# Performance work log

Hardware: AMD Instinct MI355X
Metric: run time of the kernel (lower is better)

Reference implementation:

```python
import jax, jax.numpy as jnp
import numpy as np

WH, WW = 8, 8            # window_size
N_TOK = WH * WW          # tokens per window = 64
DIM = 128
HEADS = 4
HEAD_DIM = DIM // HEADS  # 32
B_WIN = 4096             # batch * num_windows
EPS = 1e-6


def _swin_relative_index():
    # standard Swin relative_position_index, shape (N, N), values in [0, (2Wh-1)*(2Ww-1))
    coords = np.stack(np.meshgrid(np.arange(WH), np.arange(WW), indexing='ij'))  # (2, Wh, Ww)
    coords = coords.reshape(2, -1)                                               # (2, N)
    rel = coords[:, :, None] - coords[:, None, :]                                # (2, N, N)
    rel = rel.transpose(1, 2, 0).astype(np.int32)                                # (N, N, 2)
    rel[..., 0] += WH - 1
    rel[..., 1] += WW - 1
    rel[..., 0] *= 2 * WW - 1
    return rel.sum(-1)                                                           # (N, N)


def _coords_grid():
    # normalized relative coordinate table, shape ((2Wh-1)*(2Ww-1), 2) in [-1, 1]
    rh = np.arange(-(WH - 1), WH, dtype=np.float32) / max(WH - 1, 1)
    rw = np.arange(-(WW - 1), WW, dtype=np.float32) / max(WW - 1, 1)
    return np.stack(np.meshgrid(rh, rw, indexing='ij'), -1).reshape(-1, 2)


def setup_inputs() -> dict:
    key = jax.random.key(0)
    ks = jax.random.split(key, 8)
    s = 0.02
    return {
        'x':       jax.random.normal(ks[0], (B_WIN, N_TOK, DIM), jnp.float32),
        'W_qkv':   jax.random.normal(ks[1], (DIM, 3 * DIM), jnp.float32) * s,
        'W_proj':  jax.random.normal(ks[2], (DIM, DIM), jnp.float32) * s,
        'b_proj':  jnp.zeros((DIM,), jnp.float32),
        'cpb_w1':  jax.random.normal(ks[3], (2, 512), jnp.float32) * s,
        'cpb_b1':  jnp.zeros((512,), jnp.float32),
        'cpb_w2':  jax.random.normal(ks[4], (512, HEADS), jnp.float32) * s,
        'h_times':   jnp.float32(2.0),
        'pow_para':  jnp.float32(0.0),
        'ws_scalar': jnp.float32(1.0),
        'ws_scalar2': jnp.float32(2.0),
        'rel_index': jnp.asarray(_swin_relative_index()),          # (N, N) int32
        'coords':    jnp.asarray(_coords_grid()),                  # (225, 2) float32
    }


def reference(x, W_qkv, W_proj, b_proj, cpb_w1, cpb_b1, cpb_w2,
              h_times, pow_para, ws_scalar, ws_scalar2, rel_index, coords):
    B, N, C = x.shape
    scale = HEAD_DIM ** -0.5

    # qkv projection (bias=False), split into heads
    qkv = (x @ W_qkv).reshape(B, N, 3, HEADS, HEAD_DIM)
    qkv = jnp.transpose(qkv, (2, 0, 3, 1, 4))           # (3, B, H, N, hd)
    q, k, v = qkv[0], qkv[1], qkv[2]

    attn = jnp.einsum('bhnd,bhmd->bhnm', q, k) * scale  # (B, H, N, N)

    # dynamic position bias: parametrized coord transform -> small MLP -> gather
    ht = jax.nn.softplus(h_times)
    pp = jax.nn.sigmoid(pow_para)
    ws = jax.nn.softplus(ws_scalar) / jax.nn.softplus(ws_scalar2)
    t = coords * ht                                      # (225, 2)
    t = jnp.sign(t) * (jnp.abs(t) + EPS) ** pp * ws      # pow_mode coord warp
    bias_table = jax.nn.relu(t @ cpb_w1 + cpb_b1) @ cpb_w2   # (225, H)
    bias = bias_table[rel_index]                         # (N, N, H)
    attn = attn + jnp.transpose(bias, (2, 0, 1))[None]   # (B, H, N, N)

    attn = jax.nn.softmax(attn, axis=-1)
    out = jnp.einsum('bhnm,bhmd->bnhd', attn, v).reshape(B, N, C)
    return out @ W_proj + b_proj
```

## Files before the change

### kernel.cpp

```cpp
#include <hip/hip_runtime.h>
#include <hip/hip_bf16.h>

typedef __hip_bfloat16 bf16;
typedef __bf16 bf8v __attribute__((ext_vector_type(8)));
typedef float f4v __attribute__((ext_vector_type(4)));

#define WS_BIAS   0
#define WS_TABLE  32768
#define WS_QKVT   36864
#define WS_PROJT  135168
#define WS_FLAG   167936

__device__ __forceinline__ float rdf(const void* p, int i, int isbf) {
  return isbf ? __bfloat162float(((const bf16*)p)[i]) : ((const float*)p)[i];
}

__global__ void detect_dtype(const unsigned short* __restrict__ coords_raw,
                             char* __restrict__ ws) {
  *(int*)(ws + WS_FLAG) = (coords_raw[0] != 0) ? 1 : 0;
}

__global__ void prep_transpose(const void* __restrict__ Wqkv,
                               const void* __restrict__ Wproj,
                               char* __restrict__ ws) {
  int idx = blockIdx.x * 256 + threadIdx.x;
  int isbf = *(const int*)(ws + WS_FLAG);
  bf16* qt = (bf16*)(ws + WS_QKVT);
  bf16* pt = (bf16*)(ws + WS_PROJT);
  if (idx < 384 * 128) {
    int c = idx >> 7, k = idx & 127;
    qt[idx] = __float2bfloat16(rdf(Wqkv, k * 384 + c, isbf));
  } else {
    int j = idx - 384 * 128;
    int c = j >> 7, k = j & 127;
    pt[j] = __float2bfloat16(rdf(Wproj, k * 128 + c, isbf));
  }
}

__global__ void prep_table(const void* __restrict__ coords,
                           const void* __restrict__ w1,
                           const void* __restrict__ b1,
                           const void* __restrict__ w2,
                           const void* __restrict__ hts,
                           const void* __restrict__ pps,
                           const void* __restrict__ ws1,
                           const void* __restrict__ ws2,
                           char* __restrict__ ws) {
  __shared__ float red[8][4];
  const int r = blockIdx.x;
  const int j = threadIdx.x;
  const int isbf = *(const int*)(ws + WS_FLAG);
  float* table = (float*)(ws + WS_TABLE);

  float ht  = log1pf(__expf(rdf(hts, 0, isbf)));
  float pp  = 1.f / (1.f + __expf(-rdf(pps, 0, isbf)));
  float wsv = log1pf(__expf(rdf(ws1, 0, isbf))) /
              log1pf(__expf(rdf(ws2, 0, isbf)));
  float t0 = rdf(coords, 2 * r + 0, isbf) * ht;
  float t1 = rdf(coords, 2 * r + 1, isbf) * ht;
  float s0 = (t0 > 0.f) ? 1.f : ((t0 < 0.f) ? -1.f : 0.f);
  float s1 = (t1 > 0.f) ? 1.f : ((t1 < 0.f) ? -1.f : 0.f);
  float u0 = s0 * __powf(fabsf(t0) + 1e-6f, pp) * wsv;
  float u1 = s1 * __powf(fabsf(t1) + 1e-6f, pp) * wsv;

  float h = u0 * rdf(w1, j, isbf) + u1 * rdf(w1, 512 + j, isbf) + rdf(b1, j, isbf);
  h = fmaxf(h, 0.f);
  float a[4];
#pragma unroll
  for (int q = 0; q < 4; ++q) a[q] = h * rdf(w2, 4 * j + q, isbf);
#pragma unroll
  for (int off = 1; off < 64; off <<= 1)
#pragma unroll
    for (int q = 0; q < 4; ++q) a[q] += __shfl_xor(a[q], off);
  int wv = j >> 6, ln = j & 63;
  if (ln == 0) {
#pragma unroll
    for (int q = 0; q < 4; ++q) red[wv][q] = a[q];
  }
  __syncthreads();
  if (j < 4) {
    float s = 0.f;
#pragma unroll
    for (int w8 = 0; w8 < 8; ++w8) s += red[w8][j];
    table[r * 4 + j] = s;
  }
}

__global__ void prep_gather(const int* __restrict__ rel, char* __restrict__ ws) {
  int pos = blockIdx.x * 256 + threadIdx.x;
  const float* table = (const float*)(ws + WS_TABLE);
  bf16* bias = (bf16*)(ws + WS_BIAS);
  int h = pos >> 10, rest = pos & 1023;
  int mt = rest >> 8, n4 = (rest >> 6) & 3, quad = (rest >> 4) & 3, l16 = rest & 15;
  int jj = n4 * 16 + l16;
  union { uint2 u; bf16 hh[4]; } pk;
#pragma unroll
  for (int r = 0; r < 4; ++r) {
    int i = mt * 16 + quad * 4 + r;
    int rr = rel[i * 64 + jj];
    pk.hh[r] = __float2bfloat16(table[rr * 4 + h]);
  }
  *(uint2*)(bias + pos * 4) = pk.u;
}

__global__ __launch_bounds__(256, 4) void wattn_main(
    const void* __restrict__ xp,
    const char* __restrict__ ws,
    const void* __restrict__ bprojp,
    void* __restrict__ outp) {
  __shared__ alignas(16) char smem[26624];
  bf16* xls = (bf16*)smem;
  bf16* os  = (bf16*)smem;
  const int tid  = threadIdx.x;
  const int w    = tid >> 6;
  const int lane = tid & 63;
  const int l16  = lane & 15;
  const int quad = lane >> 4;
  bf16* scr = (bf16*)(smem + 17408 + w * 2304);

  const int isbf = *(const int*)(ws + WS_FLAG);
  const bf16* WqkvT  = (const bf16*)(ws + WS_QKVT);
  const bf16* WprojT = (const bf16*)(ws + WS_PROJT);
  const bf16* biasg  = (const bf16*)(ws + WS_BIAS);

  const int b = blockIdx.x;

  if (isbf) {
    const bf16* xb = (const bf16*)xp + (size_t)b * 8192;
#pragma unroll
    for (int it = 0; it < 4; ++it) {
      int e = (tid + it * 256) * 8;
      int row = e >> 7, col = e & 127;
      *(uint4*)(xls + row * 136 + col) = *(const uint4*)(xb + e);
    }
  } else {
    const float* xb = (const float*)xp + (size_t)b * 8192;
#pragma unroll
    for (int it = 0; it < 4; ++it) {
      int e = (tid + it * 256) * 8;
      int row = e >> 7, col = e & 127;
      f4v a = *(const f4v*)(xb + e);
      f4v c = *(const f4v*)(xb + e + 4);
      union { uint4 u; bf16 h[8]; } pk;
#pragma unroll
      for (int jj = 0; jj < 4; ++jj) {
        pk.h[jj]     = __float2bfloat16(a[jj]);
        pk.h[4 + jj] = __float2bfloat16(c[jj]);
      }
      *(uint4*)(xls + row * 136 + col) = pk.u;
    }
  }
  __syncthreads();

  const f4v zf = {0.f, 0.f, 0.f, 0.f};
  bf8v vf[2][2], qf[4], kf[4];

  auto run_qkv = [&](int colbase, f4v (&acc)[4][2]) {
    const bf16* Bb = WqkvT + (size_t)colbase * 128;
#pragma unroll
    for (int ks = 0; ks < 4; ++ks) {
      bf8v xk[4];
#pragma unroll
      for (int mt = 0; mt < 4; ++mt)
        xk[mt] = *(const bf8v*)(xls + (mt * 16 + l16) * 136 + ks * 32 + quad * 8);
#pragma unroll
      for (int nt = 0; nt < 2; ++nt) {
        bf8v bfr = *(const bf8v*)(Bb + (nt * 16 + l16) * 128 + ks * 32 + quad * 8);
#pragma unroll
        for (int mt = 0; mt < 4; ++mt)
          acc[mt][nt] = __builtin_amdgcn_mfma_f32_16x16x32_bf16(xk[mt], bfr, acc[mt][nt], 0, 0, 0);
      }
    }
  };

  {
    f4v acc[4][2];
#pragma unroll
    for (int mt = 0; mt < 4; ++mt) { acc[mt][0] = zf; acc[mt][1] = zf; }
    run_qkv(256 + w * 32, acc);
#pragma unroll
    for (int nt = 0; nt < 2; ++nt) {
#pragma unroll
      for (int mt = 0; mt < 4; ++mt) {
        union { uint2 u; bf16 h[4]; } pk;
#pragma unroll
        for (int r = 0; r < 4; ++r) pk.h[r] = __float2bfloat16(acc[mt][nt][r]);
        *(uint2*)(scr + l16 * 72 + mt * 16 + quad * 4) = pk.u;
      }
#pragma unroll
      for (int k2 = 0; k2 < 2; ++k2)
        vf[k2][nt] = *(const bf8v*)(scr + l16 * 72 + k2 * 32 + quad * 8);
    }
  }

  {
    f4v acc[4][2];
#pragma unroll
    for (int mt = 0; mt < 4; ++mt) { acc[mt][0] = zf; acc[mt][1] = zf; }
    run_qkv(w * 32, acc);
#pragma unroll
    for (int mt = 0; mt < 4; ++mt) {
#pragma unroll
      for (int nt = 0; nt < 2; ++nt)
#pragma unroll
        for (int r = 0; r < 4; ++r)
          scr[(quad * 4 + r) * 40 + nt * 16 + l16] = __float2bfloat16(acc[mt][nt][r]);
      qf[mt] = *(const bf8v*)(scr + l16 * 40 + quad * 8);
    }
  }

  {
    f4v acc[4][2];
#pragma unroll
    for (int mt = 0; mt < 4; ++mt) { acc[mt][0] = zf; acc[mt][1] = zf; }
    run_qkv(128 + w * 32, acc);
#pragma unroll
    for (int mt = 0; mt < 4; ++mt) {
#pragma unroll
      for (int nt = 0; nt < 2; ++nt)
#pragma unroll
        for (int r = 0; r < 4; ++r)
          scr[(quad * 4 + r) * 40 + nt * 16 + l16] = __float2bfloat16(acc[mt][nt][r]);
      kf[mt] = *(const bf8v*)(scr + l16 * 40 + quad * 8);
    }
  }

  __syncthreads();

  const float scale = 0.1767766952966369f;
  const bf16* bh = biasg + w * 4096;
  for (int mt = 0; mt < 4; ++mt) {
    f4v sc[4];
#pragma unroll
    for (int n4 = 0; n4 < 4; ++n4)
      sc[n4] = __builtin_amdgcn_mfma_f32_16x16x32_bf16(qf[mt], kf[n4], zf, 0, 0, 0);
    float p[4][4];
#pragma unroll
    for (int n4 = 0; n4 < 4; ++n4) {
      union { uint2 u; bf16 hh[4]; } bb;
      bb.u = *(const uint2*)(bh + mt * 1024 + n4 * 256 + quad * 64 + l16 * 4);
#pragma unroll
      for (int r = 0; r < 4; ++r)
        p[n4][r] = sc[n4][r] * scale + __bfloat162float(bb.hh[r]);
    }
#pragma unroll
    for (int r = 0; r < 4; ++r) {
      float m = fmaxf(fmaxf(p[0][r], p[1][r]), fmaxf(p[2][r], p[3][r]));
      m = fmaxf(m, __shfl_xor(m, 1, 16));
      m = fmaxf(m, __shfl_xor(m, 2, 16));
      m = fmaxf(m, __shfl_xor(m, 4, 16));
      m = fmaxf(m, __shfl_xor(m, 8, 16));
      float s = 0.f;
#pragma unroll
      for (int n4 = 0; n4 < 4; ++n4) { p[n4][r] = __expf(p[n4][r] - m); s += p[n4][r]; }
      s += __shfl_xor(s, 1, 16);
      s += __shfl_xor(s, 2, 16);
      s += __shfl_xor(s, 4, 16);
      s += __shfl_xor(s, 8, 16);
      float inv = __builtin_amdgcn_rcpf(s);
#pragma unroll
      for (int n4 = 0; n4 < 4; ++n4) p[n4][r] *= inv;
    }
#pragma unroll
    for (int n4 = 0; n4 < 4; ++n4)
#pragma unroll
      for (int r = 0; r < 4; ++r)
        scr[(quad * 4 + r) * 72 + n4 * 16 + l16] = __float2bfloat16(p[n4][r]);

    f4v o2[2] = {zf, zf};
#pragma unroll
    for (int k2 = 0; k2 < 2; ++k2) {
      bf8v pf = *(const bf8v*)(scr + l16 * 72 + k2 * 32 + quad * 8);
#pragma unroll
      for (int nt = 0; nt < 2; ++nt)
        o2[nt] = __builtin_amdgcn_mfma_f32_16x16x32_bf16(pf, vf[k2][nt], o2[nt], 0, 0, 0);
    }
#pragma unroll
    for (int nt = 0; nt < 2; ++nt) {
      union { uint2 u; bf16 h[4]; } pk;
#pragma unroll
      for (int r = 0; r < 4; ++r) pk.h[r] = __float2bfloat16(o2[nt][r]);
#pragma unroll
      for (int r = 0; r < 4; ++r)
        os[(mt * 16 + quad * 4 + r) * 136 + w * 32 + nt * 16 + l16] = pk.h[r];
    }
  }

  __syncthreads();

  f4v pa[4][2];
#pragma unroll
  for (int mt = 0; mt < 4; ++mt) { pa[mt][0] = zf; pa[mt][1] = zf; }
#pragma unroll
  for (int ks = 0; ks < 4; ++ks) {
    bf8v oa[4];
#pragma unroll
    for (int mt = 0; mt < 4; ++mt)
      oa[mt] = *(const bf8v*)(os + (mt * 16 + l16) * 136 + ks * 32 + quad * 8);
#pragma unroll
    for (int nt = 0; nt < 2; ++nt) {
      bf8v bfr = *(const bf8v*)(WprojT + (size_t)(w * 32 + nt * 16 + l16) * 128 + ks * 32 + quad * 8);
#pragma unroll
      for (int mt = 0; mt < 4; ++mt)
        pa[mt][nt] = __builtin_amdgcn_mfma_f32_16x16x32_bf16(oa[mt], bfr, pa[mt][nt], 0, 0, 0);
    }
  }

  if (!isbf) {
    float* ob  = (float*)outp + (size_t)b * 8192;
    float* fsf = (float*)smem;
    float bbv[2];
#pragma unroll
    for (int nt = 0; nt < 2; ++nt)
      bbv[nt] = ((const float*)bprojp)[w * 32 + nt * 16 + l16];
#pragma unroll
    for (int half = 0; half < 2; ++half) {
      __syncthreads();
#pragma unroll
      for (int nt = 0; nt < 2; ++nt) {
        int c = w * 32 + nt * 16 + l16;
#pragma unroll
        for (int m2 = 0; m2 < 2; ++m2) {
          int mt = half * 2 + m2;
#pragma unroll
          for (int r = 0; r < 4; ++r)
            fsf[(m2 * 16 + quad * 4 + r) * 132 + c] = pa[mt][nt][r] + bbv[nt];
        }
      }
      __syncthreads();
#pragma unroll
      for (int it = 0; it < 4; ++it) {
        int e4 = (tid + it * 256) * 4;
        int row = e4 >> 7, col = e4 & 127;
        *(f4v*)(ob + half * 4096 + e4) = *(const f4v*)(fsf + row * 132 + col);
      }
    }
  } else {
    __syncthreads();
#pragma unroll
    for (int nt = 0; nt < 2; ++nt) {
      int c = w * 32 + nt * 16 + l16;
      float bb = __bfloat162float(((const bf16*)bprojp)[c]);
#pragma unroll
      for (int mt = 0; mt < 4; ++mt)
#pragma unroll
        for (int r = 0; r < 4; ++r)
          xls[(mt * 16 + quad * 4 + r) * 136 + c] = __float2bfloat16(pa[mt][nt][r] + bb);
    }
    __syncthreads();
    bf16* ob = (bf16*)outp + (size_t)b * 8192;
#pragma unroll
    for (int it = 0; it < 4; ++it) {
      int e = (tid + it * 256) * 8;
      int row = e >> 7, col = e & 127;
      *(uint4*)(ob + e) = *(const uint4*)(xls + row * 136 + col);
    }
  }
}

extern "C" void kernel_launch(void* const* d_in, const int* in_sizes, int n_in,
                              void* d_out, int out_size, void* d_ws, size_t ws_size,
                              hipStream_t stream) {
  const void* x      = d_in[0];
  const void* Wqkv   = d_in[1];
  const void* Wproj  = d_in[2];
  const void* bproj  = d_in[3];
  const void* w1     = d_in[4];
  const void* b1     = d_in[5];
  const void* w2     = d_in[6];
  const void* hts    = d_in[7];
  const void* pps    = d_in[8];
  const void* ws1    = d_in[9];
  const void* ws2    = d_in[10];
  const int*  rel    = (const int*)d_in[11];
  const void* coords = d_in[12];
  char* ws  = (char*)d_ws;

  detect_dtype<<<1, 1, 0, stream>>>((const unsigned short*)coords, ws);
  prep_transpose<<<256, 256, 0, stream>>>(Wqkv, Wproj, ws);
  prep_table<<<225, 512, 0, stream>>>(coords, w1, b1, w2, hts, pps, ws1, ws2, ws);
  prep_gather<<<16, 256, 0, stream>>>(rel, ws);
  wattn_main<<<4096, 256, 0, stream>>>(x, ws, bproj, d_out);
}
```

Measured before the change: 320.1 us.

## Swizzle shared-memory layouts, shrink LDS, raise occupancy, drop dtype-detect kernel

Replaces the padded shared-memory layouts (row strides 136/72/40/132) with unpadded rows that use XOR swizzling, and shrinks the per-warp scratch so the block's LDS drops from 26 KB to 20 KB. The launch bound goes from 4 to 8 blocks per CU so more windows can be resident at once. The separate one-thread dtype-detection kernel is removed, and each kernel now reads the dtype flag from coords directly, which saves one launch. The risks are register pressure under the tighter launch bound and swizzle patterns that may not remove all bank conflicts.

```diff
diff --git a/kernel.cpp b/kernel.cpp
--- a/kernel.cpp
+++ b/kernel.cpp
@@ -9,22 +9,21 @@
 #define WS_TABLE  32768
 #define WS_QKVT   36864
 #define WS_PROJT  135168
-#define WS_FLAG   167936
 
 __device__ __forceinline__ float rdf(const void* p, int i, int isbf) {
   return isbf ? __bfloat162float(((const bf16*)p)[i]) : ((const float*)p)[i];
 }
 
-__global__ void detect_dtype(const unsigned short* __restrict__ coords_raw,
-                             char* __restrict__ ws) {
-  *(int*)(ws + WS_FLAG) = (coords_raw[0] != 0) ? 1 : 0;
+__device__ __forceinline__ int dtflag(const void* coords) {
+  return (*(const unsigned short*)coords != 0) ? 1 : 0;
 }
 
 __global__ void prep_transpose(const void* __restrict__ Wqkv,
                                const void* __restrict__ Wproj,
+                               const void* __restrict__ coords,
                                char* __restrict__ ws) {
   int idx = blockIdx.x * 256 + threadIdx.x;
-  int isbf = *(const int*)(ws + WS_FLAG);
+  int isbf = dtflag(coords);
   bf16* qt = (bf16*)(ws + WS_QKVT);
   bf16* pt = (bf16*)(ws + WS_PROJT);
   if (idx < 384 * 128) {
@@ -49,7 +48,7 @@
   __shared__ float red[8][4];
   const int r = blockIdx.x;
   const int j = threadIdx.x;
-  const int isbf = *(const int*)(ws + WS_FLAG);
+  const int isbf = dtflag(coords);
   float* table = (float*)(ws + WS_TABLE);
 
   float ht  = log1pf(__expf(rdf(hts, 0, isbf)));
@@ -103,22 +102,24 @@
   *(uint2*)(bias + pos * 4) = pk.u;
 }
 
-__global__ __launch_bounds__(256, 4) void wattn_main(
+__global__ __launch_bounds__(256, 8) void wattn_main(
     const void* __restrict__ xp,
     const char* __restrict__ ws,
     const void* __restrict__ bprojp,
+    const void* __restrict__ coords,
     void* __restrict__ outp) {
-  __shared__ alignas(16) char smem[26624];
-  bf16* xls = (bf16*)smem;
-  bf16* os  = (bf16*)smem;
+  __shared__ alignas(16) char smem[20480];
+  char* smc = smem;
   const int tid  = threadIdx.x;
   const int w    = tid >> 6;
   const int lane = tid & 63;
   const int l16  = lane & 15;
   const int quad = lane >> 4;
-  bf16* scr = (bf16*)(smem + 17408 + w * 2304);
-
-  const int isbf = *(const int*)(ws + WS_FLAG);
+  char* sb = smc + 16384 + w * 1024;
+  const int sswz = ((l16 >> 1) & 3) << 4;
+  const int rsw  = (l16 & 7) << 4;
+
+  const int isbf = dtflag(coords);
   const bf16* WqkvT  = (const bf16*)(ws + WS_QKVT);
   const bf16* WprojT = (const bf16*)(ws + WS_PROJT);
   const bf16* biasg  = (const bf16*)(ws + WS_BIAS);
@@ -130,15 +131,15 @@
 #pragma unroll
     for (int it = 0; it < 4; ++it) {
       int e = (tid + it * 256) * 8;
-      int row = e >> 7, col = e & 127;
-      *(uint4*)(xls + row * 136 + col) = *(const uint4*)(xb + e);
+      int row = e >> 7, colb = (e & 127) * 2;
+      *(uint4*)(smc + row * 256 + (colb ^ ((row & 7) << 4))) = *(const uint4*)(xb + e);
     }
   } else {
     const float* xb = (const float*)xp + (size_t)b * 8192;
 #pragma unroll
     for (int it = 0; it < 4; ++it) {
       int e = (tid + it * 256) * 8;
-      int row = e >> 7, col = e & 127;
+      int row = e >> 7, colb = (e & 127) * 2;
       f4v a = *(const f4v*)(xb + e);
       f4v c = *(const f4v*)(xb + e + 4);
       union { uint4 u; bf16 h[8]; } pk;
@@ -147,7 +148,7 @@
         pk.h[jj]     = __float2bfloat16(a[jj]);
         pk.h[4 + jj] = __float2bfloat16(c[jj]);
       }
-      *(uint4*)(xls + row * 136 + col) = pk.u;
+      *(uint4*)(smc + row * 256 + (colb ^ ((row & 7) << 4))) = pk.u;
     }
   }
   __syncthreads();
@@ -162,7 +163,7 @@
       bf8v xk[4];
 #pragma unroll
       for (int mt = 0; mt < 4; ++mt)
-        xk[mt] = *(const bf8v*)(xls + (mt * 16 + l16) * 136 + ks * 32 + quad * 8);
+        xk[mt] = *(const bf8v*)(smc + (mt * 16 + l16) * 256 + ((ks * 64 + quad * 16) ^ rsw));
 #pragma unroll
       for (int nt = 0; nt < 2; ++nt) {
         bf8v bfr = *(const bf8v*)(Bb + (nt * 16 + l16) * 128 + ks * 32 + quad * 8);
@@ -179,18 +180,19 @@
     for (int mt = 0; mt < 4; ++mt) { acc[mt][0] = zf; acc[mt][1] = zf; }
     run_qkv(256 + w * 32, acc);
 #pragma unroll
-    for (int nt = 0; nt < 2; ++nt) {
-#pragma unroll
-      for (int mt = 0; mt < 4; ++mt) {
-        union { uint2 u; bf16 h[4]; } pk;
-#pragma unroll
-        for (int r = 0; r < 4; ++r) pk.h[r] = __float2bfloat16(acc[mt][nt][r]);
-        *(uint2*)(scr + l16 * 72 + mt * 16 + quad * 4) = pk.u;
-      }
-#pragma unroll
-      for (int k2 = 0; k2 < 2; ++k2)
-        vf[k2][nt] = *(const bf8v*)(scr + l16 * 72 + k2 * 32 + quad * 8);
-    }
+    for (int nt = 0; nt < 2; ++nt)
+#pragma unroll
+      for (int k2 = 0; k2 < 2; ++k2) {
+#pragma unroll
+        for (int mh = 0; mh < 2; ++mh) {
+          int mt = k2 * 2 + mh;
+          union { uint2 u; bf16 h[4]; } pk;
+#pragma unroll
+          for (int r = 0; r < 4; ++r) pk.h[r] = __float2bfloat16(acc[mt][nt][r]);
+          *(uint2*)(sb + l16 * 64 + ((mh * 32 + quad * 8) ^ sswz)) = pk.u;
+        }
+        vf[k2][nt] = *(const bf8v*)(sb + l16 * 64 + ((quad * 16) ^ sswz));
+      }
   }
 
   {
@@ -204,8 +206,10 @@
       for (int nt = 0; nt < 2; ++nt)
 #pragma unroll
         for (int r = 0; r < 4; ++r)
-          scr[(quad * 4 + r) * 40 + nt * 16 + l16] = __float2bfloat16(acc[mt][nt][r]);
-      qf[mt] = *(const bf8v*)(scr + l16 * 40 + quad * 8);
+          *(bf16*)(sb + (quad * 4 + r) * 64 +
+                   ((nt * 32 + l16 * 2) ^ ((((quad * 2) + (r >> 1)) & 3) << 4))) =
+              __float2bfloat16(acc[mt][nt][r]);
+      qf[mt] = *(const bf8v*)(sb + l16 * 64 + ((quad * 16) ^ sswz));
     }
   }
 
@@ -220,8 +224,10 @@
       for (int nt = 0; nt < 2; ++nt)
 #pragma unroll
         for (int r = 0; r < 4; ++r)
-          scr[(quad * 4 + r) * 40 + nt * 16 + l16] = __float2bfloat16(acc[mt][nt][r]);
-      kf[mt] = *(const bf8v*)(scr + l16 * 40 + quad * 8);
+          *(bf16*)(sb + (quad * 4 + r) * 64 +
+                   ((nt * 32 + l16 * 2) ^ ((((quad * 2) + (r >> 1)) & 3) << 4))) =
+              __float2bfloat16(acc[mt][nt][r]);
+      kf[mt] = *(const bf8v*)(sb + l16 * 64 + ((quad * 16) ^ sswz));
     }
   }
 
@@ -261,16 +267,19 @@
 #pragma unroll
       for (int n4 = 0; n4 < 4; ++n4) p[n4][r] *= inv;
     }
-#pragma unroll
-    for (int n4 = 0; n4 < 4; ++n4)
-#pragma unroll
-      for (int r = 0; r < 4; ++r)
-        scr[(quad * 4 + r) * 72 + n4 * 16 + l16] = __float2bfloat16(p[n4][r]);
-
     f4v o2[2] = {zf, zf};
 #pragma unroll
     for (int k2 = 0; k2 < 2; ++k2) {
-      bf8v pf = *(const bf8v*)(scr + l16 * 72 + k2 * 32 + quad * 8);
+#pragma unroll
+      for (int nh = 0; nh < 2; ++nh) {
+        int n4 = k2 * 2 + nh;
+#pragma unroll
+        for (int r = 0; r < 4; ++r)
+          *(bf16*)(sb + (quad * 4 + r) * 64 +
+                   ((nh * 32 + l16 * 2) ^ ((((quad * 2) + (r >> 1)) & 3) << 4))) =
+              __float2bfloat16(p[n4][r]);
+      }
+      bf8v pf = *(const bf8v*)(sb + l16 * 64 + ((quad * 16) ^ sswz));
 #pragma unroll
       for (int nt = 0; nt < 2; ++nt)
         o2[nt] = __builtin_amdgcn_mfma_f32_16x16x32_bf16(pf, vf[k2][nt], o2[nt], 0, 0, 0);
@@ -281,8 +290,11 @@
 #pragma unroll
       for (int r = 0; r < 4; ++r) pk.h[r] = __float2bfloat16(o2[nt][r]);
 #pragma unroll
-      for (int r = 0; r < 4; ++r)
-        os[(mt * 16 + quad * 4 + r) * 136 + w * 32 + nt * 16 + l16] = pk.h[r];
+      for (int r = 0; r < 4; ++r) {
+        int row = mt * 16 + quad * 4 + r;
+        *(bf16*)(smc + row * 256 +
+                 (((w * 32 + nt * 16 + l16) * 2) ^ ((row & 7) << 4))) = pk.h[r];
+      }
     }
   }
 
@@ -296,7 +308,7 @@
     bf8v oa[4];
 #pragma unroll
     for (int mt = 0; mt < 4; ++mt)
-      oa[mt] = *(const bf8v*)(os + (mt * 16 + l16) * 136 + ks * 32 + quad * 8);
+      oa[mt] = *(const bf8v*)(smc + (mt * 16 + l16) * 256 + ((ks * 64 + quad * 16) ^ rsw));
 #pragma unroll
     for (int nt = 0; nt < 2; ++nt) {
       bf8v bfr = *(const bf8v*)(WprojT + (size_t)(w * 32 + nt * 16 + l16) * 128 + ks * 32 + quad * 8);
@@ -307,8 +319,7 @@
   }
 
   if (!isbf) {
-    float* ob  = (float*)outp + (size_t)b * 8192;
-    float* fsf = (float*)smem;
+    float* ob = (float*)outp + (size_t)b * 8192;
     float bbv[2];
 #pragma unroll
     for (int nt = 0; nt < 2; ++nt)
@@ -323,16 +334,20 @@
         for (int m2 = 0; m2 < 2; ++m2) {
           int mt = half * 2 + m2;
 #pragma unroll
-          for (int r = 0; r < 4; ++r)
-            fsf[(m2 * 16 + quad * 4 + r) * 132 + c] = pa[mt][nt][r] + bbv[nt];
+          for (int r = 0; r < 4; ++r) {
+            int row = m2 * 16 + quad * 4 + r;
+            *(float*)(smc + row * 512 + ((c * 4) ^ ((row & 7) << 4))) =
+                pa[mt][nt][r] + bbv[nt];
+          }
         }
       }
       __syncthreads();
 #pragma unroll
       for (int it = 0; it < 4; ++it) {
         int e4 = (tid + it * 256) * 4;
-        int row = e4 >> 7, col = e4 & 127;
-        *(f4v*)(ob + half * 4096 + e4) = *(const f4v*)(fsf + row * 132 + col);
+        int row = e4 >> 7, colb = (e4 & 127) * 4;
+        *(f4v*)(ob + half * 4096 + e4) =
+            *(const f4v*)(smc + row * 512 + (colb ^ ((row & 7) << 4)));
       }
     }
   } else {
@@ -344,16 +359,19 @@
 #pragma unroll
       for (int mt = 0; mt < 4; ++mt)
 #pragma unroll
-        for (int r = 0; r < 4; ++r)
-          xls[(mt * 16 + quad * 4 + r) * 136 + c] = __float2bfloat16(pa[mt][nt][r] + bb);
+        for (int r = 0; r < 4; ++r) {
+          int row = mt * 16 + quad * 4 + r;
+          *(bf16*)(smc + row * 256 + ((c * 2) ^ ((row & 7) << 4))) =
+              __float2bfloat16(pa[mt][nt][r] + bb);
+        }
     }
     __syncthreads();
     bf16* ob = (bf16*)outp + (size_t)b * 8192;
 #pragma unroll
     for (int it = 0; it < 4; ++it) {
       int e = (tid + it * 256) * 8;
-      int row = e >> 7, col = e & 127;
-      *(uint4*)(ob + e) = *(const uint4*)(xls + row * 136 + col);
+      int row = e >> 7, colb = (e & 127) * 2;
+      *(uint4*)(ob + e) = *(const uint4*)(smc + row * 256 + (colb ^ ((row & 7) << 4)));
     }
   }
 }
@@ -376,9 +394,8 @@
   const void* coords = d_in[12];
   char* ws  = (char*)d_ws;
 
-  detect_dtype<<<1, 1, 0, stream>>>((const unsigned short*)coords, ws);
-  prep_transpose<<<256, 256, 0, stream>>>(Wqkv, Wproj, ws);
+  prep_transpose<<<256, 256, 0, stream>>>(Wqkv, Wproj, coords, ws);
   prep_table<<<225, 512, 0, stream>>>(coords, w1, b1, w2, hts, pps, ws1, ws2, ws);
   prep_gather<<<16, 256, 0, stream>>>(rel, ws);
-  wattn_main<<<4096, 256, 0, stream>>>(x, ws, bproj, d_out);
-}
+  wattn_main<<<4096, 256, 0, stream>>>(x, ws, bproj, coords, d_out);
+}
```

After: 543.2 us. 1.7x slower.

## Transpose score MFMA, use register bpermute for P, drop dtype detect kernel

Applied to the files above, without the earlier changes.

Swaps the MFMA operands so scores come out transposed: each lane holds one query row's column slice, and the softmax max and sum reduce across quads with two shuffles instead of four per row. The probability matrix is repacked into the PV operand through ds_bpermute, replacing the round trip through LDS scratch, and the output is stored as packed 8-byte writes. The bias gather layout is transposed to match, bias loads are hoisted ahead of the MFMAs, and the separate dtype-detect kernel launch is removed by reading coords directly in each kernel. The added cost is extra bpermute and select instructions per tile.

```diff
diff --git a/kernel.cpp b/kernel.cpp
--- a/kernel.cpp
+++ b/kernel.cpp
@@ -9,22 +9,28 @@
 #define WS_TABLE  32768
 #define WS_QKVT   36864
 #define WS_PROJT  135168
-#define WS_FLAG   167936
 
 __device__ __forceinline__ float rdf(const void* p, int i, int isbf) {
   return isbf ? __bfloat162float(((const bf16*)p)[i]) : ((const float*)p)[i];
 }
 
-__global__ void detect_dtype(const unsigned short* __restrict__ coords_raw,
-                             char* __restrict__ ws) {
-  *(int*)(ws + WS_FLAG) = (coords_raw[0] != 0) ? 1 : 0;
+__device__ __forceinline__ int dtflag(const void* coords) {
+  return (*(const unsigned short*)coords != 0) ? 1 : 0;
+}
+
+__device__ __forceinline__ unsigned pkbf(float a, float b) {
+  union { bf16 h[2]; unsigned u; } t;
+  t.h[0] = __float2bfloat16(a);
+  t.h[1] = __float2bfloat16(b);
+  return t.u;
 }
 
 __global__ void prep_transpose(const void* __restrict__ Wqkv,
                                const void* __restrict__ Wproj,
+                               const void* __restrict__ coords,
                                char* __restrict__ ws) {
   int idx = blockIdx.x * 256 + threadIdx.x;
-  int isbf = *(const int*)(ws + WS_FLAG);
+  int isbf = dtflag(coords);
   bf16* qt = (bf16*)(ws + WS_QKVT);
   bf16* pt = (bf16*)(ws + WS_PROJT);
   if (idx < 384 * 128) {
@@ -49,7 +55,7 @@
   __shared__ float red[8][4];
   const int r = blockIdx.x;
   const int j = threadIdx.x;
-  const int isbf = *(const int*)(ws + WS_FLAG);
+  const int isbf = dtflag(coords);
   float* table = (float*)(ws + WS_TABLE);
 
   float ht  = log1pf(__expf(rdf(hts, 0, isbf)));
@@ -92,12 +98,10 @@
   bf16* bias = (bf16*)(ws + WS_BIAS);
   int h = pos >> 10, rest = pos & 1023;
   int mt = rest >> 8, n4 = (rest >> 6) & 3, quad = (rest >> 4) & 3, l16 = rest & 15;
-  int jj = n4 * 16 + l16;
   union { uint2 u; bf16 hh[4]; } pk;
 #pragma unroll
   for (int r = 0; r < 4; ++r) {
-    int i = mt * 16 + quad * 4 + r;
-    int rr = rel[i * 64 + jj];
+    int rr = rel[(mt * 16 + l16) * 64 + (n4 * 16 + quad * 4 + r)];
     pk.hh[r] = __float2bfloat16(table[rr * 4 + h]);
   }
   *(uint2*)(bias + pos * 4) = pk.u;
@@ -107,6 +111,7 @@
     const void* __restrict__ xp,
     const char* __restrict__ ws,
     const void* __restrict__ bprojp,
+    const void* __restrict__ coords,
     void* __restrict__ outp) {
   __shared__ alignas(16) char smem[26624];
   bf16* xls = (bf16*)smem;
@@ -118,7 +123,7 @@
   const int quad = lane >> 4;
   bf16* scr = (bf16*)(smem + 17408 + w * 2304);
 
-  const int isbf = *(const int*)(ws + WS_FLAG);
+  const int isbf = dtflag(coords);
   const bf16* WqkvT  = (const bf16*)(ws + WS_QKVT);
   const bf16* WprojT = (const bf16*)(ws + WS_PROJT);
   const bf16* biasg  = (const bf16*)(ws + WS_BIAS);
@@ -229,60 +234,75 @@
 
   const float scale = 0.1767766952966369f;
   const bf16* bh = biasg + w * 4096;
+  const bool hi2 = (quad >> 1) != 0;
+  const int a0 = ((quad & 1) * 32 + l16) * 4;
   for (int mt = 0; mt < 4; ++mt) {
+    uint2 bbu[4];
+#pragma unroll
+    for (int n4 = 0; n4 < 4; ++n4)
+      bbu[n4] = *(const uint2*)(bh + mt * 1024 + n4 * 256 + quad * 64 + l16 * 4);
     f4v sc[4];
 #pragma unroll
     for (int n4 = 0; n4 < 4; ++n4)
-      sc[n4] = __builtin_amdgcn_mfma_f32_16x16x32_bf16(qf[mt], kf[n4], zf, 0, 0, 0);
+      sc[n4] = __builtin_amdgcn_mfma_f32_16x16x32_bf16(kf[n4], qf[mt], zf, 0, 0, 0);
     float p[4][4];
 #pragma unroll
     for (int n4 = 0; n4 < 4; ++n4) {
-      union { uint2 u; bf16 hh[4]; } bb;
-      bb.u = *(const uint2*)(bh + mt * 1024 + n4 * 256 + quad * 64 + l16 * 4);
+      union { uint2 u; bf16 hh[4]; } bb; bb.u = bbu[n4];
 #pragma unroll
       for (int r = 0; r < 4; ++r)
         p[n4][r] = sc[n4][r] * scale + __bfloat162float(bb.hh[r]);
     }
-#pragma unroll
-    for (int r = 0; r < 4; ++r) {
-      float m = fmaxf(fmaxf(p[0][r], p[1][r]), fmaxf(p[2][r], p[3][r]));
-      m = fmaxf(m, __shfl_xor(m, 1, 16));
-      m = fmaxf(m, __shfl_xor(m, 2, 16));
-      m = fmaxf(m, __shfl_xor(m, 4, 16));
-      m = fmaxf(m, __shfl_xor(m, 8, 16));
-      float s = 0.f;
-#pragma unroll
-      for (int n4 = 0; n4 < 4; ++n4) { p[n4][r] = __expf(p[n4][r] - m); s += p[n4][r]; }
-      s += __shfl_xor(s, 1, 16);
-      s += __shfl_xor(s, 2, 16);
-      s += __shfl_xor(s, 4, 16);
-      s += __shfl_xor(s, 8, 16);
-      float inv = __builtin_amdgcn_rcpf(s);
-#pragma unroll
-      for (int n4 = 0; n4 < 4; ++n4) p[n4][r] *= inv;
-    }
-#pragma unroll
-    for (int n4 = 0; n4 < 4; ++n4)
-#pragma unroll
-      for (int r = 0; r < 4; ++r)
-        scr[(quad * 4 + r) * 72 + n4 * 16 + l16] = __float2bfloat16(p[n4][r]);
-
+    float m0 = fmaxf(fmaxf(p[0][0], p[0][1]), fmaxf(p[0][2], p[0][3]));
+    float m1 = fmaxf(fmaxf(p[1][0], p[1][1]), fmaxf(p[1][2], p[1][3]));
+    float m2 = fmaxf(fmaxf(p[2][0], p[2][1]), fmaxf(p[2][2], p[2][3]));
+    float m3 = fmaxf(fmaxf(p[3][0], p[3][1]), fmaxf(p[3][2], p[3][3]));
+    float mx = fmaxf(fmaxf(m0, m1), fmaxf(m2, m3));
+    mx = fmaxf(mx, __shfl_xor(mx, 16));
+    mx = fmaxf(mx, __shfl_xor(mx, 32));
+    float s = 0.f;
+#pragma unroll
+    for (int n4 = 0; n4 < 4; ++n4) {
+      float t0 = __expf(p[n4][0] - mx), t1 = __expf(p[n4][1] - mx);
+      float t2 = __expf(p[n4][2] - mx), t3 = __expf(p[n4][3] - mx);
+      p[n4][0] = t0; p[n4][1] = t1; p[n4][2] = t2; p[n4][3] = t3;
+      s += (t0 + t1) + (t2 + t3);
+    }
+    s += __shfl_xor(s, 16);
+    s += __shfl_xor(s, 32);
+    float inv = __builtin_amdgcn_rcpf(s);
+    unsigned pk32[4][2];
+#pragma unroll
+    for (int n4 = 0; n4 < 4; ++n4) {
+      pk32[n4][0] = pkbf(p[n4][0] * inv, p[n4][1] * inv);
+      pk32[n4][1] = pkbf(p[n4][2] * inv, p[n4][3] * inv);
+    }
     f4v o2[2] = {zf, zf};
 #pragma unroll
-    for (int k2 = 0; k2 < 2; ++k2) {
-      bf8v pf = *(const bf8v*)(scr + l16 * 72 + k2 * 32 + quad * 8);
+    for (int ks = 0; ks < 2; ++ks) {
+      unsigned w0a = __builtin_amdgcn_ds_bpermute(a0,      (int)pk32[2 * ks][0]);
+      unsigned w0b = __builtin_amdgcn_ds_bpermute(a0,      (int)pk32[2 * ks + 1][0]);
+      unsigned w1a = __builtin_amdgcn_ds_bpermute(a0,      (int)pk32[2 * ks][1]);
+      unsigned w1b = __builtin_amdgcn_ds_bpermute(a0,      (int)pk32[2 * ks + 1][1]);
+      unsigned w2a = __builtin_amdgcn_ds_bpermute(a0 + 64, (int)pk32[2 * ks][0]);
+      unsigned w2b = __builtin_amdgcn_ds_bpermute(a0 + 64, (int)pk32[2 * ks + 1][0]);
+      unsigned w3a = __builtin_amdgcn_ds_bpermute(a0 + 64, (int)pk32[2 * ks][1]);
+      unsigned w3b = __builtin_amdgcn_ds_bpermute(a0 + 64, (int)pk32[2 * ks + 1][1]);
+      union { unsigned u[4]; bf8v v; } pf;
+      pf.u[0] = hi2 ? w0b : w0a;
+      pf.u[1] = hi2 ? w1b : w1a;
+      pf.u[2] = hi2 ? w2b : w2a;
+      pf.u[3] = hi2 ? w3b : w3a;
 #pragma unroll
       for (int nt = 0; nt < 2; ++nt)
-        o2[nt] = __builtin_amdgcn_mfma_f32_16x16x32_bf16(pf, vf[k2][nt], o2[nt], 0, 0, 0);
+        o2[nt] = __builtin_amdgcn_mfma_f32_16x16x32_bf16(vf[ks][nt], pf.v, o2[nt], 0, 0, 0);
     }
 #pragma unroll
     for (int nt = 0; nt < 2; ++nt) {
       union { uint2 u; bf16 h[4]; } pk;
 #pragma unroll
       for (int r = 0; r < 4; ++r) pk.h[r] = __float2bfloat16(o2[nt][r]);
-#pragma unroll
-      for (int r = 0; r < 4; ++r)
-        os[(mt * 16 + quad * 4 + r) * 136 + w * 32 + nt * 16 + l16] = pk.h[r];
+      *(uint2*)(os + (mt * 16 + l16) * 136 + w * 32 + nt * 16 + quad * 4) = pk.u;
     }
   }
 
@@ -376,9 +396,8 @@
   const void* coords = d_in[12];
   char* ws  = (char*)d_ws;
 
-  detect_dtype<<<1, 1, 0, stream>>>((const unsigned short*)coords, ws);
-  prep_transpose<<<256, 256, 0, stream>>>(Wqkv, Wproj, ws);
+  prep_transpose<<<256, 256, 0, stream>>>(Wqkv, Wproj, coords, ws);
   prep_table<<<225, 512, 0, stream>>>(coords, w1, b1, w2, hts, pps, ws1, ws2, ws);
   prep_gather<<<16, 256, 0, stream>>>(rel, ws);
-  wattn_main<<<4096, 256, 0, stream>>>(x, ws, bproj, d_out);
-}
+  wattn_main<<<4096, 256, 0, stream>>>(x, ws, bproj, coords, d_out);
+}
```

Measured after the change: 304.9 us. 4.7% less time.
